# Kernel optimization log

Hardware: AMD Instinct MI355X
Metric: run time of the kernel (lower is better)

## Reference

```python
import jax, jax.numpy as jnp
import numpy as np

N_NODES = 100000
N_FULL = 1000000
N_EDGES = 500000
D_FEAT = 128


def setup_inputs() -> dict:
    key = jax.random.key(0)
    k1, k2, k3, k4, k5, k6 = jax.random.split(key, 6)
    h = jax.random.normal(k1, (N_NODES, D_FEAT), dtype=jnp.float32)
    # popularity counts >= 1 so ipw = 1/pop is well-behaved
    pop = jax.random.uniform(k2, (N_NODES, 1), dtype=jnp.float32) + 1.0
    bias = jax.random.normal(k3, (N_FULL,), dtype=jnp.float32)
    src = jax.random.randint(k4, (N_EDGES,), 0, N_NODES, dtype=jnp.int64)
    dst = jax.random.randint(k5, (N_EDGES,), 0, N_NODES, dtype=jnp.int64)
    nid = jax.random.randint(k6, (N_NODES,), 0, N_FULL, dtype=jnp.int64)
    return {"h": h, "pop": pop, "bias": bias, "src": src, "dst": dst, "nid": nid}


def reference(h, pop, bias, src, dst, nid):
    # u_dot_v('h','h','s'): per-edge dot product of endpoint features -> [E]
    s = jnp.sum(h[src] * h[dst], axis=-1)
    # ipw = 1/pop per node ([N,1]); u_dot_v('ipw','ipw') -> product of scalars per edge
    ipw = 1.0 / pop  # [N, 1]
    ipw_score = jnp.sum(ipw[src] * ipw[dst], axis=-1)  # [E]
    # bias gather-add: bias indexed by full-graph node ids of edge endpoints
    s = s + bias[nid[src]] + bias[nid[dst]]
    pair_score = s * ipw_score
    return pair_score
```

## Files before the change

kernel.cpp:

```cpp
#include <hip/hip_runtime.h>
#include <hip/hip_fp16.h>


union H8 {
    float4  f4;
    __half2 h2[4];
};

__device__ inline float dot8(const H8& a, const H8& b) {
    float s = 0.0f;
#pragma unroll
    for (int k = 0; k < 4; ++k) {
        float2 fa = __half22float2(a.h2[k]);
        float2 fb = __half22float2(b.h2[k]);
        s += fa.x * fb.x + fa.y * fb.y;
    }
    return s;
}

__global__ __launch_bounds__(256) void prep_kernel(
    const float* __restrict__ h,
    __half*      __restrict__ h16,
    const float* __restrict__ pop,
    const float* __restrict__ bias,
    const int*   __restrict__ nid,
    float2*      __restrict__ nodeinfo,
    int n_elems,
    int n_nodes,
    int conv_blocks)
{
    if (blockIdx.x < (unsigned)conv_blocks) {
        int i = blockIdx.x * blockDim.x + threadIdx.x;
        int base = i * 8;
        if (base < n_elems) {
            const float4 f0 = *reinterpret_cast<const float4*>(h + base);
            const float4 f1 = *reinterpret_cast<const float4*>(h + base + 4);
            H8 o;
            o.h2[0] = __floats2half2_rn(f0.x, f0.y);
            o.h2[1] = __floats2half2_rn(f0.z, f0.w);
            o.h2[2] = __floats2half2_rn(f1.x, f1.y);
            o.h2[3] = __floats2half2_rn(f1.z, f1.w);
            *reinterpret_cast<float4*>(h16 + base) = o.f4;
        }
    } else {
        int i = (blockIdx.x - conv_blocks) * blockDim.x + threadIdx.x;
        if (i < n_nodes) {
            nodeinfo[i] = make_float2(1.0f / pop[i], bias[nid[i]]);
        }
    }
}

__global__ __launch_bounds__(256) void edge_score_f16_kernel(
    const __half* __restrict__ h16,
    const float2* __restrict__ nodeinfo,
    const int*    __restrict__ src,
    const int*    __restrict__ dst,
    float*        __restrict__ out,
    int n_edges)
{
    const int gtid = blockIdx.x * blockDim.x + threadIdx.x;
    const int e    = gtid >> 3;
    const int lane = threadIdx.x & 7;
    if (e >= n_edges) return;

    const int si = __builtin_nontemporal_load(src + e);
    const int di = __builtin_nontemporal_load(dst + e);

    const __half* ra = h16 + (size_t)si * 128 + lane * 8;
    const __half* rb = h16 + (size_t)di * 128 + lane * 8;

    H8 a0, a1, b0, b1;
    a0.f4 = *reinterpret_cast<const float4*>(ra);
    a1.f4 = *reinterpret_cast<const float4*>(ra + 64);
    b0.f4 = *reinterpret_cast<const float4*>(rb);
    b1.f4 = *reinterpret_cast<const float4*>(rb + 64);

    float part = dot8(a0, b0) + dot8(a1, b1);

    part += __shfl_xor(part, 1);
    part += __shfl_xor(part, 2);
    part += __shfl_xor(part, 4);

    if (lane == 0) {
        const float2 ns = nodeinfo[si];
        const float2 nd = nodeinfo[di];
        __builtin_nontemporal_store((part + ns.y + nd.y) * (ns.x * nd.x), out + e);
    }
}


__global__ __launch_bounds__(256) void edge_score_fallback_kernel(
    const float* __restrict__ h,
    const float* __restrict__ pop,
    const float* __restrict__ bias,
    const int*   __restrict__ src,
    const int*   __restrict__ dst,
    const int*   __restrict__ nid,
    float*       __restrict__ out,
    int n_edges)
{
    const int gtid = blockIdx.x * blockDim.x + threadIdx.x;
    const int e    = gtid >> 4;
    const int lane = threadIdx.x & 15;
    if (e >= n_edges) return;

    const int si = src[e];
    const int di = dst[e];
    const float* ra = h + (size_t)si * 128 + lane * 8;
    const float* rb = h + (size_t)di * 128 + lane * 8;
    const float4 a0 = *reinterpret_cast<const float4*>(ra);
    const float4 a1 = *reinterpret_cast<const float4*>(ra + 4);
    const float4 b0 = *reinterpret_cast<const float4*>(rb);
    const float4 b1 = *reinterpret_cast<const float4*>(rb + 4);

    float part = a0.x * b0.x + a0.y * b0.y + a0.z * b0.z + a0.w * b0.w
               + a1.x * b1.x + a1.y * b1.y + a1.z * b1.z + a1.w * b1.w;

    part += __shfl_xor(part, 1);
    part += __shfl_xor(part, 2);
    part += __shfl_xor(part, 4);
    part += __shfl_xor(part, 8);

    if (lane == 0) {
        const float ipw = (1.0f / pop[si]) * (1.0f / pop[di]);
        const float bb  = bias[nid[si]] + bias[nid[di]];
        out[e] = (part + bb) * ipw;
    }
}

extern "C" void kernel_launch(void* const* d_in, const int* in_sizes, int n_in,
                              void* d_out, int out_size, void* d_ws, size_t ws_size,
                              hipStream_t stream) {
    const float* h    = (const float*)d_in[0];
    const float* pop  = (const float*)d_in[1];
    const float* bias = (const float*)d_in[2];
    const int*   src  = (const int*)d_in[3];
    const int*   dst  = (const int*)d_in[4];
    const int*   nid  = (const int*)d_in[5];
    float*       out  = (float*)d_out;

    const int n_edges = in_sizes[3];
    const int n_nodes = in_sizes[1];
    const int n_elems = in_sizes[0];

    auto align256 = [](size_t x) { return (x + 255) & ~(size_t)255; };
    const size_t h16_bytes  = align256((size_t)n_elems * sizeof(__half));
    const size_t info_bytes = align256((size_t)n_nodes * sizeof(float2));

    if (ws_size >= h16_bytes + info_bytes) {
        __half* h16      = (__half*)d_ws;
        float2* nodeinfo = (float2*)((char*)d_ws + h16_bytes);

        const int conv_blocks = (n_elems / 8 + 255) / 256;
        const int prep_blocks = (n_nodes + 255) / 256;
        prep_kernel<<<conv_blocks + prep_blocks, 256, 0, stream>>>(
            h, h16, pop, bias, nid, nodeinfo, n_elems, n_nodes, conv_blocks);

        int grid = ((n_edges * 8) + 255) / 256;
        edge_score_f16_kernel<<<grid, 256, 0, stream>>>(h16, nodeinfo, src, dst,
                                                        out, n_edges);
    } else {
        int grid = ((n_edges * 16) + 255) / 256;
        edge_score_fallback_kernel<<<grid, 256, 0, stream>>>(h, pop, bias, src, dst, nid,
                                                             out, n_edges);
    }
}
```

Measured before the change: 54.90 us.

## Partition edges by source-node range before scoring to improve cache locality

Adds a counting sort that buckets edges into 8 partitions by source node range. It uses a per-block histogram, a single-block scan, and a scatter into packed (src, dst, edge id) records. The scoring kernel then interleaves blocks across partitions so concurrently running blocks touch a smaller slice of source rows. The aim is to raise L2/MALL hit rates on the half-precision feature gathers. The cost is three extra kernel launches and roughly 16 bytes of records written and read per edge. The existing fallback path also drops its nontemporal loads and stores.

```diff
diff --git a/kernel.cpp b/kernel.cpp
--- a/kernel.cpp
+++ b/kernel.cpp
@@ -1,6 +1,11 @@
 #include <hip/hip_runtime.h>
 #include <hip/hip_fp16.h>
 
+
+#define NPART 8
+#define SCAN_THREADS 1024
+#define SCAN_PER_THREAD 16
+#define SCAN_CAP (SCAN_THREADS * SCAN_PER_THREAD)
 
 union H8 {
     float4  f4;
@@ -25,9 +30,7 @@
     const float* __restrict__ bias,
     const int*   __restrict__ nid,
     float2*      __restrict__ nodeinfo,
-    int n_elems,
-    int n_nodes,
-    int conv_blocks)
+    int n_elems, int n_nodes, int conv_blocks)
 {
     if (blockIdx.x < (unsigned)conv_blocks) {
         int i = blockIdx.x * blockDim.x + threadIdx.x;
@@ -50,6 +53,130 @@
     }
 }
 
+__global__ __launch_bounds__(256) void blockcount_kernel(
+    const int* __restrict__ src,
+    unsigned*  __restrict__ blockcounts,
+    int n_edges, int nb, int part_div)
+{
+    __shared__ unsigned hist[NPART];
+    if (threadIdx.x < NPART) hist[threadIdx.x] = 0u;
+    __syncthreads();
+
+    int e = blockIdx.x * 256 + threadIdx.x;
+    if (e < n_edges) {
+        int p = src[e] / part_div;
+        atomicAdd(&hist[p], 1u);
+    }
+    __syncthreads();
+
+    if (threadIdx.x < NPART)
+        blockcounts[threadIdx.x * nb + blockIdx.x] = hist[threadIdx.x];
+}
+
+__global__ __launch_bounds__(SCAN_THREADS) void scan_kernel(
+    const unsigned* __restrict__ counts,
+    unsigned*       __restrict__ offs,
+    int n)
+{
+    __shared__ unsigned part[SCAN_THREADS];
+    const int t = threadIdx.x;
+    const int base = t * SCAN_PER_THREAD;
+
+    unsigned v[SCAN_PER_THREAD];
+    unsigned s = 0;
+#pragma unroll
+    for (int i = 0; i < SCAN_PER_THREAD; ++i) {
+        unsigned x = (base + i < n) ? counts[base + i] : 0u;
+        v[i] = s;
+        s += x;
+    }
+    part[t] = s;
+    __syncthreads();
+
+    for (int off = 1; off < SCAN_THREADS; off <<= 1) {
+        unsigned u = (t >= off) ? part[t - off] : 0u;
+        __syncthreads();
+        part[t] += u;
+        __syncthreads();
+    }
+
+    unsigned tb = (t == 0) ? 0u : part[t - 1];
+#pragma unroll
+    for (int i = 0; i < SCAN_PER_THREAD; ++i) {
+        if (base + i < n) offs[base + i] = tb + v[i];
+    }
+}
+
+__global__ __launch_bounds__(256) void scatter_kernel(
+    const int* __restrict__ src,
+    const int* __restrict__ dst,
+    const unsigned* __restrict__ offs,
+    int4*      __restrict__ rec,
+    int n_edges, int nb, int part_div)
+{
+    __shared__ unsigned cur[NPART];
+    if (threadIdx.x < NPART)
+        cur[threadIdx.x] = offs[threadIdx.x * nb + blockIdx.x];
+    __syncthreads();
+
+    int e = blockIdx.x * 256 + threadIdx.x;
+    if (e < n_edges) {
+        int si = src[e];
+        int p  = si / part_div;
+        unsigned pos = atomicAdd(&cur[p], 1u);
+        rec[pos] = make_int4(si, dst[e], e, 0);
+    }
+}
+
+__global__ __launch_bounds__(256) void edge_score_part_kernel(
+    const __half*   __restrict__ h16,
+    const float2*   __restrict__ nodeinfo,
+    const int4*     __restrict__ rec,
+    const unsigned* __restrict__ offs,
+    float*          __restrict__ out,
+    int n_edges, int nb)
+{
+    const int p = blockIdx.x & (NPART - 1);
+    const int c = blockIdx.x >> 3;
+
+    const unsigned pstart = offs[p * nb];
+    const unsigned pend   = (p + 1 < NPART) ? offs[(p + 1) * nb]
+                                            : (unsigned)n_edges;
+
+    const int grp  = threadIdx.x >> 3;
+    const int lane = threadIdx.x & 7;
+
+    const unsigned k = pstart + (unsigned)c * 32u + (unsigned)grp;
+    if (k >= pend) return;
+
+    const int4 r  = rec[k];
+    const int  si = r.x;
+    const int  di = r.y;
+
+    const __half* ra = h16 + (size_t)si * 128 + lane * 8;
+    const __half* rb = h16 + (size_t)di * 128 + lane * 8;
+
+    H8 a0, a1, b0, b1;
+    a0.f4 = *reinterpret_cast<const float4*>(ra);
+    a1.f4 = *reinterpret_cast<const float4*>(ra + 64);
+    b0.f4 = *reinterpret_cast<const float4*>(rb);
+    b1.f4 = *reinterpret_cast<const float4*>(rb + 64);
+
+    float part = dot8(a0, b0) + dot8(a1, b1);
+
+    part += __shfl_xor(part, 1);
+    part += __shfl_xor(part, 2);
+    part += __shfl_xor(part, 4);
+
+    if (lane == 0) {
+        const float2 ns = nodeinfo[si];
+        const float2 nd = nodeinfo[di];
+        __builtin_nontemporal_store((part + ns.y + nd.y) * (ns.x * nd.x),
+                                    out + r.z);
+    }
+}
+
+
 __global__ __launch_bounds__(256) void edge_score_f16_kernel(
     const __half* __restrict__ h16,
     const float2* __restrict__ nodeinfo,
@@ -63,9 +190,8 @@
     const int lane = threadIdx.x & 7;
     if (e >= n_edges) return;
 
-    const int si = __builtin_nontemporal_load(src + e);
-    const int di = __builtin_nontemporal_load(dst + e);
-
+    const int si = src[e];
+    const int di = dst[e];
     const __half* ra = h16 + (size_t)si * 128 + lane * 8;
     const __half* rb = h16 + (size_t)di * 128 + lane * 8;
 
@@ -84,10 +210,9 @@
     if (lane == 0) {
         const float2 ns = nodeinfo[si];
         const float2 nd = nodeinfo[di];
-        __builtin_nontemporal_store((part + ns.y + nd.y) * (ns.x * nd.x), out + e);
-    }
-}
-
+        out[e] = (part + ns.y + nd.y) * (ns.x * nd.x);
+    }
+}
 
 __global__ __launch_bounds__(256) void edge_score_fallback_kernel(
     const float* __restrict__ h,
@@ -147,13 +272,45 @@
     const size_t h16_bytes  = align256((size_t)n_elems * sizeof(__half));
     const size_t info_bytes = align256((size_t)n_nodes * sizeof(float2));
 
-    if (ws_size >= h16_bytes + info_bytes) {
+    const int nb       = (n_edges + 255) / 256;
+    const int n_flat   = NPART * nb;
+    const int part_div = (n_nodes + NPART - 1) / NPART;
+
+    const size_t cnt_bytes = align256((size_t)n_flat * sizeof(unsigned));
+    const size_t rec_bytes = align256((size_t)n_edges * sizeof(int4));
+    const size_t full_bytes = h16_bytes + info_bytes + 2 * cnt_bytes + rec_bytes;
+
+    if (ws_size >= full_bytes && n_flat <= SCAN_CAP) {
+        char* wp = (char*)d_ws;
+        __half*   h16      = (__half*)wp;    wp += h16_bytes;
+        float2*   nodeinfo = (float2*)wp;    wp += info_bytes;
+        unsigned* counts   = (unsigned*)wp;  wp += cnt_bytes;
+        unsigned* offs     = (unsigned*)wp;  wp += cnt_bytes;
+        int4*     rec      = (int4*)wp;
+
+        const int conv_blocks = (n_elems / 8 + 255) / 256;
+        const int info_blocks = (n_nodes + 255) / 256;
+        prep_kernel<<<conv_blocks + info_blocks, 256, 0, stream>>>(
+            h, h16, pop, bias, nid, nodeinfo, n_elems, n_nodes, conv_blocks);
+
+        blockcount_kernel<<<nb, 256, 0, stream>>>(src, counts, n_edges, nb, part_div);
+
+        scan_kernel<<<1, SCAN_THREADS, 0, stream>>>(counts, offs, n_flat);
+
+        scatter_kernel<<<nb, 256, 0, stream>>>(src, dst, offs, rec,
+                                               n_edges, nb, part_div);
+
+        const int epb  = 256 / 8;
+        const int bpp  = (n_edges + NPART * epb - 1) / (NPART * epb) + 256;
+        edge_score_part_kernel<<<bpp * NPART, 256, 0, stream>>>(
+            h16, nodeinfo, rec, offs, out, n_edges, nb);
+    } else if (ws_size >= h16_bytes + info_bytes) {
         __half* h16      = (__half*)d_ws;
         float2* nodeinfo = (float2*)((char*)d_ws + h16_bytes);
 
         const int conv_blocks = (n_elems / 8 + 255) / 256;
-        const int prep_blocks = (n_nodes + 255) / 256;
-        prep_kernel<<<conv_blocks + prep_blocks, 256, 0, stream>>>(
+        const int info_blocks = (n_nodes + 255) / 256;
+        prep_kernel<<<conv_blocks + info_blocks, 256, 0, stream>>>(
             h, h16, pop, bias, nid, nodeinfo, n_elems, n_nodes, conv_blocks);
 
         int grid = ((n_edges * 8) + 255) / 256;
```

New measurement: 75.16 us. 1.37x slower.
